# Performance work log

Measured on AMD Instinct MI355X. Metric: run time of the kernel, lower is better.

Reference implementation:

```python
import jax, jax.numpy as jnp
import numpy as np

B, L, D, F, T = 32, 768, 256, 256, 3072
_EPS = 1e-5


def _layernorm(h, g, b):
    mu = jnp.mean(h, axis=-1, keepdims=True)
    var = jnp.var(h, axis=-1, keepdims=True)
    return (h - mu) * jax.lax.rsqrt(var + _EPS) * g + b


def _conv1d(h, w, b):
    # h: [B, L, Cin], w: [K, Cin, Cout] (HIO), padding=1 matches torch Conv1d(padding=1)
    return jax.lax.conv_general_dilated(h, w, (1,), [(1, 1)], dimension_numbers=('NHC', 'HIO', 'NHC')) + b


def setup_inputs() -> dict:
    key = jax.random.key(0)
    ks = jax.random.split(key, 6)
    return {
        'x': jax.random.normal(ks[0], (B, L, D), jnp.float32),
        'target': jax.random.randint(ks[1], (B, L), 0, 4, jnp.int32),
        'mel_max_length': T,
        'conv1_w': jax.random.normal(ks[2], (3, D, F), jnp.float32) * 0.05,
        'conv1_b': jnp.zeros((F,), jnp.float32),
        'ln1_g': jnp.ones((F,), jnp.float32),
        'ln1_b': jnp.zeros((F,), jnp.float32),
        'conv2_w': jax.random.normal(ks[3], (3, F, F), jnp.float32) * 0.05,
        'conv2_b': jnp.zeros((F,), jnp.float32),
        'ln2_g': jnp.ones((F,), jnp.float32),
        'ln2_b': jnp.zeros((F,), jnp.float32),
        'lin_w': jax.random.normal(ks[4], (F, 1), jnp.float32) * 0.05,
        'lin_b': jnp.zeros((1,), jnp.float32),
    }


def reference(x, target, mel_max_length, conv1_w, conv1_b, ln1_g, ln1_b,
              conv2_w, conv2_b, ln2_g, ln2_b, lin_w, lin_b):
    alpha = 1.0
    # DurationPredictor: conv -> relu -> LN -> conv -> relu -> LN -> linear (dropout=0)
    h = _layernorm(jax.nn.relu(_conv1d(x, conv1_w, conv1_b)), ln1_g, ln1_b)
    h = _layernorm(jax.nn.relu(_conv1d(h, conv2_w, conv2_b)), ln2_g, ln2_b)
    dp_out = (h @ lin_w + lin_b)[..., 0]                       # [B, L]
    durations = jnp.exp(dp_out) * alpha                        # [B, L] float
    # Training branch: durations come from target
    dpo = jnp.round(target.astype(jnp.float32) * alpha).astype(jnp.int32)  # [B, L]
    # LR: alignment @ x realized as cumulative-duration searchsorted + gather
    cum = jnp.cumsum(dpo, axis=1)                              # [B, L]
    t = jnp.arange(mel_max_length, dtype=jnp.int32)            # [T]
    idx = jax.vmap(lambda c: jnp.searchsorted(c, t, side='right'))(cum)  # [B, T]
    mask = (t[None, :] < cum[:, -1:]).astype(x.dtype)          # [B, T] zero past total frames
    out = jnp.take_along_axis(x, jnp.clip(idx, 0, x.shape[1] - 1)[:, :, None], axis=1)
    out = out * mask[:, :, None]                               # [B, T, D]
    return (out, dpo, durations)
```

## Files before the change

kernel.cpp:

```cpp
#include <hip/hip_runtime.h>
#include <hip/hip_bf16.h>
#include <math.h>

#define BB 32
#define LL 768
#define DD 256
#define FF 256
#define TT 3072
#define MT 48
#define PAD 262
#define A1R 66

typedef __attribute__((ext_vector_type(8))) short bf16x8;
typedef __attribute__((ext_vector_type(4))) float f32x4;

__device__ inline unsigned short f2b(float f) {
    union { float f; unsigned u; } v; v.f = f;
    unsigned r = (v.u + 0x7FFF + ((v.u >> 16) & 1)) >> 16;
    return (unsigned short)r;
}

__device__ inline unsigned cvt_pk_bf16(float lo, float hi) {
    unsigned r;
    asm("v_cvt_pk_bf16_f32 %0, %1, %2" : "=v"(r) : "v"(lo), "v"(hi));
    return r;
}

#define DPP_ROR_ADD(v, ctrl)                                                   \
    v += __int_as_float(__builtin_amdgcn_update_dpp(                           \
        0, __float_as_int(v), ctrl, 0xF, 0xF, false))

__device__ inline void red16_pair(float& a, float& b) {
    DPP_ROR_ADD(a, 0x128); DPP_ROR_ADD(b, 0x128);
    DPP_ROR_ADD(a, 0x124); DPP_ROR_ADD(b, 0x124);
    DPP_ROR_ADD(a, 0x122); DPP_ROR_ADD(b, 0x122);
    DPP_ROR_ADD(a, 0x121); DPP_ROR_ADD(b, 0x121);
}

__device__ inline float red16_one(float a) {
    DPP_ROR_ADD(a, 0x128);
    DPP_ROR_ADD(a, 0x124);
    DPP_ROR_ADD(a, 0x122);
    DPP_ROR_ADD(a, 0x121);
    return a;
}

__global__ __launch_bounds__(256) void prep_scan_kernel(
    const float* __restrict__ w1, const float* __restrict__ w2,
    unsigned short* __restrict__ wQ1, unsigned short* __restrict__ wQ2,
    const int* __restrict__ target,
    float* __restrict__ out_dpo,
    int* __restrict__ idx_map)
{
    __shared__ int tsum[256];
    const int tid = threadIdx.x;

    if (blockIdx.x < 48) {
        const int layer = blockIdx.x / 24;
        const int s  = blockIdx.x % 24;
        const int kc = s >> 3, c8 = s & 7;
        const float* __restrict__ w = layer ? w2 : w1;
        unsigned short* __restrict__ o = (layer ? wQ2 : wQ1) + s * 8192 + tid * 32;
        const int n = tid;

        alignas(16) unsigned short tmp[32];
#pragma unroll
        for (int q = 0; q < 4; ++q)
#pragma unroll
            for (int j = 0; j < 8; ++j) {
                const int cin = c8 * 32 + q * 8 + j;
                tmp[q * 8 + j] = f2b(w[((size_t)(kc * 256 + cin)) * 256 + n]);
            }
#pragma unroll
        for (int i = 0; i < 4; ++i)
            *reinterpret_cast<uint4*>(o + i * 8) = *reinterpret_cast<const uint4*>(tmp + i * 8);
        return;
    }

    const int b = blockIdx.x - 48;

    const int l = 3 * tid;
    const int v0 = target[b * LL + l];
    const int v1 = target[b * LL + l + 1];
    const int v2 = target[b * LL + l + 2];
    out_dpo[b * LL + l]     = (float)v0;
    out_dpo[b * LL + l + 1] = (float)v1;
    out_dpo[b * LL + l + 2] = (float)v2;

    const int s0 = v0, s1 = v0 + v1, s2 = v0 + v1 + v2;
    tsum[tid] = s2;
    __syncthreads();
    for (int off = 1; off < 256; off <<= 1) {
        int xq = (tid >= off) ? tsum[tid - off] : 0;
        __syncthreads();
        tsum[tid] += xq;
        __syncthreads();
    }
    const int excl = tsum[tid] - s2;

    for (int t = tid; t < TT; t += 256) idx_map[b * TT + t] = -1;
    __syncthreads();

    const int c0 = excl + s0, c1 = excl + s1, c2 = excl + s2;
    for (int t = excl; t < c0 && t < TT; ++t) idx_map[b * TT + t] = l;
    for (int t = c0;   t < c1 && t < TT; ++t) idx_map[b * TT + t] = l + 1;
    for (int t = c1;   t < c2 && t < TT; ++t) idx_map[b * TT + t] = l + 2;
}

__global__ __launch_bounds__(256, 2) void fused_dp_kernel(
    const float* __restrict__ x,
    const unsigned short* __restrict__ wQ1,
    const unsigned short* __restrict__ wQ2,
    const float* __restrict__ c1b, const float* __restrict__ g1, const float* __restrict__ b1,
    const float* __restrict__ c2b, const float* __restrict__ g2, const float* __restrict__ b2,
    const float* __restrict__ lw,  const float* __restrict__ lb,
    float* __restrict__ out_dur)
{
    __shared__ union {
        unsigned short A1[A1R * PAD];
        unsigned short h2[50 * PAD];
    } sm;
    __shared__ float red[4][4][4][4][2];
    __shared__ float redp[4][3][4][4];
    __shared__ float fin[50][2];

    const int tid  = threadIdx.x;
    const int b    = blockIdx.x / (LL / MT);
    const int l0   = (blockIdx.x % (LL / MT)) * MT;
    const int wave = tid >> 6, lane = tid & 63;
    const int quad = lane >> 4, l16 = lane & 15;

    int   cols[4];
    float c1bv[4], g1v[4], b1v[4], c2bv[4], g2v[4], b2v[4], lwv[4];
#pragma unroll
    for (int nt = 0; nt < 4; ++nt) {
        const int c = wave * 64 + nt * 16 + l16;
        cols[nt] = c;
        c1bv[nt] = c1b[c]; g1v[nt] = g1[c]; b1v[nt] = b1[c];
        c2bv[nt] = c2b[c]; g2v[nt] = g2[c]; b2v[nt] = b2[c];
        lwv[nt]  = lw[c];
    }
    const float lbv = lb[0];

    {
        float4 v0[7], v1[7];
        int lr[7];
#pragma unroll
        for (int k = 0; k < 7; ++k) {
            const int q  = tid + (k << 8);
            const int ar = q >> 5;
            const int l  = l0 - 2 + ar;
            lr[k] = (ar < 52 && l >= 0 && l < LL) ? l : -1;
            if (lr[k] >= 0) {
                const float* pp = x + ((size_t)b * LL + lr[k]) * DD + (q & 31) * 8;
                v0[k] = *reinterpret_cast<const float4*>(pp);
                v1[k] = *reinterpret_cast<const float4*>(pp + 4);
            }
        }
#pragma unroll
        for (int k = 0; k < 7; ++k) {
            const int q  = tid + (k << 8);
            const int ar = q >> 5;
            uint4 uu = {0u, 0u, 0u, 0u};
            if (lr[k] >= 0) {
                uu.x = cvt_pk_bf16(v0[k].x, v0[k].y);
                uu.y = cvt_pk_bf16(v0[k].z, v0[k].w);
                uu.z = cvt_pk_bf16(v1[k].x, v1[k].y);
                uu.w = cvt_pk_bf16(v1[k].z, v1[k].w);
            }
            *reinterpret_cast<uint4*>(&sm.A1[ar * PAD + (q & 31) * 8]) = uu;
        }
        for (int q = tid; q < 320; q += 256) {
            const int ar = 56 + (q >> 5);
            uint4 z = {0u, 0u, 0u, 0u};
            *reinterpret_cast<uint4*>(&sm.A1[ar * PAD + (q & 31) * 8]) = z;
        }
    }
    __syncthreads();

    f32x4 acc1[4][4] = {};
    {
        bf16x8 aE[4], bE[4], aO[4], bO[4];
        auto ld1 = [&](bf16x8* a, bf16x8* bf, int s) {
            const int kc = s >> 3, c8 = s & 7;
#pragma unroll
            for (int nt = 0; nt < 4; ++nt)
                bf[nt] = *reinterpret_cast<const bf16x8*>(
                    wQ1 + (size_t)s * 8192 + cols[nt] * 32 + quad * 8);
#pragma unroll
            for (int mt = 0; mt < 4; ++mt)
                a[mt] = *reinterpret_cast<const bf16x8*>(
                    &sm.A1[(16 * mt + l16 + kc) * PAD + c8 * 32 + quad * 8]);
        };
        auto mm1 = [&](bf16x8* a, bf16x8* bf) {
            __builtin_amdgcn_s_setprio(1);
#pragma unroll
            for (int mt = 0; mt < 4; ++mt)
#pragma unroll
                for (int nt = 0; nt < 4; ++nt)
                    acc1[mt][nt] = __builtin_amdgcn_mfma_f32_16x16x32_bf16(
                        a[mt], bf[nt], acc1[mt][nt], 0, 0, 0);
            __builtin_amdgcn_s_setprio(0);
        };
        ld1(aE, bE, 0);
        for (int s = 0; s < 24; s += 2) {
            ld1(aO, bO, s + 1);
            mm1(aE, bE);
            if (s + 2 < 24) ld1(aE, bE, s + 2);
            mm1(aO, bO);
        }
    }
    __syncthreads();

#pragma unroll
    for (int mt = 0; mt < 4; ++mt)
#pragma unroll
        for (int r = 0; r < 4; ++r) {
            float s1 = 0.f, s2 = 0.f;
#pragma unroll
            for (int nt = 0; nt < 4; ++nt) {
                const float v = fmaxf(acc1[mt][nt][r] + c1bv[nt], 0.f);
                s1 += v; s2 += v * v;
            }
            red16_pair(s1, s2);
            if (l16 == 0) { red[wave][mt][quad][r][0] = s1; red[wave][mt][quad][r][1] = s2; }
        }
    __syncthreads();
    if (tid < 50) {
        const int mt = tid >> 4, q = (tid >> 2) & 3, r = tid & 3;
        const float s1 = red[0][mt][q][r][0] + red[1][mt][q][r][0]
                       + red[2][mt][q][r][0] + red[3][mt][q][r][0];
        const float s2 = red[0][mt][q][r][1] + red[1][mt][q][r][1]
                       + red[2][mt][q][r][1] + red[3][mt][q][r][1];
        const float mu  = s1 * (1.f / 256.f);
        const float var = s2 * (1.f / 256.f) - mu * mu;
        fin[tid][0] = mu;
        fin[tid][1] = rsqrtf(var + 1e-5f);
    }
    __syncthreads();

#pragma unroll
    for (int mt = 0; mt < 4; ++mt)
#pragma unroll
        for (int r = 0; r < 4; ++r) {
            const int rho = 16 * mt + quad * 4 + r;
            if (rho < 50) {
                const int gr = l0 - 1 + rho;
                const float mu = fin[rho][0], rstd = fin[rho][1];
#pragma unroll
                for (int nt = 0; nt < 4; ++nt) {
                    unsigned short hv = 0;
                    if (gr >= 0 && gr < LL) {
                        const float v = fmaxf(acc1[mt][nt][r] + c1bv[nt], 0.f);
                        hv = f2b((v - mu) * rstd * g1v[nt] + b1v[nt]);
                    }
                    sm.h2[rho * PAD + cols[nt]] = hv;
                }
            }
        }
    __syncthreads();

    f32x4 acc2[3][4] = {};
    {
        bf16x8 aE[3], bE[4], aO[3], bO[4];
        auto ld2 = [&](bf16x8* a, bf16x8* bf, int s) {
            const int kc = s >> 3, c8 = s & 7;
#pragma unroll
            for (int nt = 0; nt < 4; ++nt)
                bf[nt] = *reinterpret_cast<const bf16x8*>(
                    wQ2 + (size_t)s * 8192 + cols[nt] * 32 + quad * 8);
#pragma unroll
            for (int mt = 0; mt < 3; ++mt)
                a[mt] = *reinterpret_cast<const bf16x8*>(
                    &sm.h2[(16 * mt + l16 + kc) * PAD + c8 * 32 + quad * 8]);
        };
        auto mm2 = [&](bf16x8* a, bf16x8* bf) {
            __builtin_amdgcn_s_setprio(1);
#pragma unroll
            for (int mt = 0; mt < 3; ++mt)
#pragma unroll
                for (int nt = 0; nt < 4; ++nt)
                    acc2[mt][nt] = __builtin_amdgcn_mfma_f32_16x16x32_bf16(
                        a[mt], bf[nt], acc2[mt][nt], 0, 0, 0);
            __builtin_amdgcn_s_setprio(0);
        };
        ld2(aE, bE, 0);
        for (int s = 0; s < 24; s += 2) {
            ld2(aO, bO, s + 1);
            mm2(aE, bE);
            if (s + 2 < 24) ld2(aE, bE, s + 2);
            mm2(aO, bO);
        }
    }

#pragma unroll
    for (int mt = 0; mt < 3; ++mt)
#pragma unroll
        for (int r = 0; r < 4; ++r) {
            float s1 = 0.f, s2 = 0.f;
#pragma unroll
            for (int nt = 0; nt < 4; ++nt) {
                const float v = fmaxf(acc2[mt][nt][r] + c2bv[nt], 0.f);
                s1 += v; s2 += v * v;
            }
            red16_pair(s1, s2);
            if (l16 == 0) { red[wave][mt][quad][r][0] = s1; red[wave][mt][quad][r][1] = s2; }
        }
    __syncthreads();
    if (tid < MT) {
        const int mt = tid >> 4, q = (tid >> 2) & 3, r = tid & 3;
        const float s1 = red[0][mt][q][r][0] + red[1][mt][q][r][0]
                       + red[2][mt][q][r][0] + red[3][mt][q][r][0];
        const float s2 = red[0][mt][q][r][1] + red[1][mt][q][r][1]
                       + red[2][mt][q][r][1] + red[3][mt][q][r][1];
        const float mu  = s1 * (1.f / 256.f);
        const float var = s2 * (1.f / 256.f) - mu * mu;
        fin[tid][0] = mu;
        fin[tid][1] = rsqrtf(var + 1e-5f);
    }
    __syncthreads();

#pragma unroll
    for (int mt = 0; mt < 3; ++mt)
#pragma unroll
        for (int r = 0; r < 4; ++r) {
            const int rho = 16 * mt + quad * 4 + r;
            const float mu = fin[rho][0], rstd = fin[rho][1];
            float p = 0.f;
#pragma unroll
            for (int nt = 0; nt < 4; ++nt) {
                const float v = fmaxf(acc2[mt][nt][r] + c2bv[nt], 0.f);
                p += ((v - mu) * rstd * g2v[nt] + b2v[nt]) * lwv[nt];
            }
            p = red16_one(p);
            if (l16 == 0) redp[wave][mt][quad][r] = p;
        }
    __syncthreads();
    if (tid < MT) {
        const int mt = tid >> 4, q = (tid >> 2) & 3, r = tid & 3;
        const float dp = redp[0][mt][q][r] + redp[1][mt][q][r]
                       + redp[2][mt][q][r] + redp[3][mt][q][r] + lbv;
        out_dur[(size_t)b * LL + l0 + tid] = expf(dp);
    }
}

__global__ __launch_bounds__(256) void gather_kernel(
    const float* __restrict__ x,
    const int* __restrict__ idx_map,
    float* __restrict__ out)
{
    const int wv = threadIdx.x >> 6, lane = threadIdx.x & 63;
    const int row = blockIdx.x * 4 + wv;
    const int b = row / TT, t = row - b * TT;
    const int idx = idx_map[b * TT + t];
    f32x4 val = {0.f, 0.f, 0.f, 0.f};
    if (idx >= 0)
        val = *reinterpret_cast<const f32x4*>(x + ((size_t)(b * LL + idx)) * DD + lane * 4);
    __builtin_nontemporal_store(val, reinterpret_cast<f32x4*>(out) + (size_t)row * (DD / 4) + lane);
}

extern "C" void kernel_launch(void* const* d_in, const int* in_sizes, int n_in,
                              void* d_out, int out_size, void* d_ws, size_t ws_size,
                              hipStream_t stream)
{
    const float* x      = (const float*)d_in[0];
    const int*   target = (const int*)  d_in[1];
    const float* c1w = (const float*)d_in[3];
    const float* c1b = (const float*)d_in[4];
    const float* g1  = (const float*)d_in[5];
    const float* b1  = (const float*)d_in[6];
    const float* c2w = (const float*)d_in[7];
    const float* c2b = (const float*)d_in[8];
    const float* g2  = (const float*)d_in[9];
    const float* b2  = (const float*)d_in[10];
    const float* lw  = (const float*)d_in[11];
    const float* lb  = (const float*)d_in[12];

    float* out0    = (float*)d_out;
    float* out_dpo = out0 + (size_t)BB * TT * DD;
    float* out_dur = out_dpo + (size_t)BB * LL;

    char* ws = (char*)d_ws;
    unsigned short* wQ1 = (unsigned short*)ws;                 ws += (size_t)24 * 8192 * 2;
    unsigned short* wQ2 = (unsigned short*)ws;                 ws += (size_t)24 * 8192 * 2;
    int* idx_map        = (int*)ws;

    prep_scan_kernel<<<48 + BB, 256, 0, stream>>>(
        c1w, c2w, wQ1, wQ2, target, out_dpo, idx_map);

    fused_dp_kernel<<<BB * (LL / MT), 256, 0, stream>>>(
        x, wQ1, wQ2, c1b, g1, b1, c2b, g2, b2, lw, lb, out_dur);

    gather_kernel<<<BB * TT / 4, 256, 0, stream>>>(x, idx_map, out0);
}
```

Before: 193.3 us.

## Load conv1 A operands directly from global, drop LDS staging and prefetch conv2 weights

The first conv's input tile is no longer staged through shared memory. Each wave loads fp32 rows of x straight from global inside the K loop, converts them to bf16 in registers and feeds them to MFMA with software pipelining. This removes the LDS write, a barrier and the shared union. The second conv's weight loads are issued before the barrier and the loop is re-pipelined, so weights arrive earlier. The cost is redundant global reads of x across the four waves and more registers in flight, which could reduce occupancy.

```diff
diff --git a/kernel.cpp b/kernel.cpp
--- a/kernel.cpp
+++ b/kernel.cpp
@@ -9,7 +9,6 @@
 #define TT 3072
 #define MT 48
 #define PAD 262
-#define A1R 66
 
 typedef __attribute__((ext_vector_type(8))) short bf16x8;
 typedef __attribute__((ext_vector_type(4))) float f32x4;
@@ -116,10 +115,7 @@
     const float* __restrict__ lw,  const float* __restrict__ lb,
     float* __restrict__ out_dur)
 {
-    __shared__ union {
-        unsigned short A1[A1R * PAD];
-        unsigned short h2[50 * PAD];
-    } sm;
+    __shared__ unsigned short h2[50 * PAD];
     __shared__ float red[4][4][4][4][2];
     __shared__ float redp[4][3][4][4];
     __shared__ float fin[50][2];
@@ -142,55 +138,39 @@
     }
     const float lbv = lb[0];
 
-    {
-        float4 v0[7], v1[7];
-        int lr[7];
-#pragma unroll
-        for (int k = 0; k < 7; ++k) {
-            const int q  = tid + (k << 8);
-            const int ar = q >> 5;
-            const int l  = l0 - 2 + ar;
-            lr[k] = (ar < 52 && l >= 0 && l < LL) ? l : -1;
-            if (lr[k] >= 0) {
-                const float* pp = x + ((size_t)b * LL + lr[k]) * DD + (q & 31) * 8;
-                v0[k] = *reinterpret_cast<const float4*>(pp);
-                v1[k] = *reinterpret_cast<const float4*>(pp + 4);
-            }
-        }
-#pragma unroll
-        for (int k = 0; k < 7; ++k) {
-            const int q  = tid + (k << 8);
-            const int ar = q >> 5;
-            uint4 uu = {0u, 0u, 0u, 0u};
-            if (lr[k] >= 0) {
-                uu.x = cvt_pk_bf16(v0[k].x, v0[k].y);
-                uu.y = cvt_pk_bf16(v0[k].z, v0[k].w);
-                uu.z = cvt_pk_bf16(v1[k].x, v1[k].y);
-                uu.w = cvt_pk_bf16(v1[k].z, v1[k].w);
-            }
-            *reinterpret_cast<uint4*>(&sm.A1[ar * PAD + (q & 31) * 8]) = uu;
-        }
-        for (int q = tid; q < 320; q += 256) {
-            const int ar = 56 + (q >> 5);
-            uint4 z = {0u, 0u, 0u, 0u};
-            *reinterpret_cast<uint4*>(&sm.A1[ar * PAD + (q & 31) * 8]) = z;
-        }
-    }
-    __syncthreads();
-
     f32x4 acc1[4][4] = {};
     {
         bf16x8 aE[4], bE[4], aO[4], bO[4];
-        auto ld1 = [&](bf16x8* a, bf16x8* bf, int s) {
+        float4 r0[4], r1[4];
+        auto issue1 = [&](bf16x8* bf, int s) {
             const int kc = s >> 3, c8 = s & 7;
+#pragma unroll
+            for (int mt = 0; mt < 4; ++mt) {
+                const int ar = 16 * mt + l16 + kc;
+                const int l  = l0 - 2 + ar;
+                float4 z = {0.f, 0.f, 0.f, 0.f};
+                r0[mt] = z; r1[mt] = z;
+                if (ar < 52 && l >= 0 && l < LL) {
+                    const float* pp = x + ((size_t)b * LL + l) * DD + c8 * 32 + quad * 8;
+                    r0[mt] = *reinterpret_cast<const float4*>(pp);
+                    r1[mt] = *reinterpret_cast<const float4*>(pp + 4);
+                }
+            }
 #pragma unroll
             for (int nt = 0; nt < 4; ++nt)
                 bf[nt] = *reinterpret_cast<const bf16x8*>(
                     wQ1 + (size_t)s * 8192 + cols[nt] * 32 + quad * 8);
-#pragma unroll
-            for (int mt = 0; mt < 4; ++mt)
-                a[mt] = *reinterpret_cast<const bf16x8*>(
-                    &sm.A1[(16 * mt + l16 + kc) * PAD + c8 * 32 + quad * 8]);
+        };
+        auto cvt1 = [&](bf16x8* a) {
+#pragma unroll
+            for (int mt = 0; mt < 4; ++mt) {
+                union { unsigned u[4]; bf16x8 v; } t;
+                t.u[0] = cvt_pk_bf16(r0[mt].x, r0[mt].y);
+                t.u[1] = cvt_pk_bf16(r0[mt].z, r0[mt].w);
+                t.u[2] = cvt_pk_bf16(r1[mt].x, r1[mt].y);
+                t.u[3] = cvt_pk_bf16(r1[mt].z, r1[mt].w);
+                a[mt] = t.v;
+            }
         };
         auto mm1 = [&](bf16x8* a, bf16x8* bf) {
             __builtin_amdgcn_s_setprio(1);
@@ -202,15 +182,17 @@
                         a[mt], bf[nt], acc1[mt][nt], 0, 0, 0);
             __builtin_amdgcn_s_setprio(0);
         };
-        ld1(aE, bE, 0);
+        issue1(bE, 0);
+        cvt1(aE);
         for (int s = 0; s < 24; s += 2) {
-            ld1(aO, bO, s + 1);
+            issue1(bO, s + 1);
             mm1(aE, bE);
-            if (s + 2 < 24) ld1(aE, bE, s + 2);
+            cvt1(aO);
+            if (s + 2 < 24) issue1(bE, s + 2);
             mm1(aO, bO);
-        }
-    }
-    __syncthreads();
+            if (s + 2 < 24) cvt1(aE);
+        }
+    }
 
 #pragma unroll
     for (int mt = 0; mt < 4; ++mt)
@@ -254,26 +236,31 @@
                         const float v = fmaxf(acc1[mt][nt][r] + c1bv[nt], 0.f);
                         hv = f2b((v - mu) * rstd * g1v[nt] + b1v[nt]);
                     }
-                    sm.h2[rho * PAD + cols[nt]] = hv;
+                    h2[rho * PAD + cols[nt]] = hv;
                 }
             }
         }
+
+    bf16x8 aE2[3], bE2[4], aO2[3], bO2[4];
+    auto ldb2 = [&](bf16x8* bf, int s) {
+#pragma unroll
+        for (int nt = 0; nt < 4; ++nt)
+            bf[nt] = *reinterpret_cast<const bf16x8*>(
+                wQ2 + (size_t)s * 8192 + cols[nt] * 32 + quad * 8);
+    };
+    auto lda2 = [&](bf16x8* a, int s) {
+        const int kc = s >> 3, c8 = s & 7;
+#pragma unroll
+        for (int mt = 0; mt < 3; ++mt)
+            a[mt] = *reinterpret_cast<const bf16x8*>(
+                &h2[(16 * mt + l16 + kc) * PAD + c8 * 32 + quad * 8]);
+    };
+    ldb2(bE2, 0);
+    ldb2(bO2, 1);
     __syncthreads();
 
     f32x4 acc2[3][4] = {};
     {
-        bf16x8 aE[3], bE[4], aO[3], bO[4];
-        auto ld2 = [&](bf16x8* a, bf16x8* bf, int s) {
-            const int kc = s >> 3, c8 = s & 7;
-#pragma unroll
-            for (int nt = 0; nt < 4; ++nt)
-                bf[nt] = *reinterpret_cast<const bf16x8*>(
-                    wQ2 + (size_t)s * 8192 + cols[nt] * 32 + quad * 8);
-#pragma unroll
-            for (int mt = 0; mt < 3; ++mt)
-                a[mt] = *reinterpret_cast<const bf16x8*>(
-                    &sm.h2[(16 * mt + l16 + kc) * PAD + c8 * 32 + quad * 8]);
-        };
         auto mm2 = [&](bf16x8* a, bf16x8* bf) {
             __builtin_amdgcn_s_setprio(1);
 #pragma unroll
@@ -284,12 +271,13 @@
                         a[mt], bf[nt], acc2[mt][nt], 0, 0, 0);
             __builtin_amdgcn_s_setprio(0);
         };
-        ld2(aE, bE, 0);
+        lda2(aE2, 0);
         for (int s = 0; s < 24; s += 2) {
-            ld2(aO, bO, s + 1);
-            mm2(aE, bE);
-            if (s + 2 < 24) ld2(aE, bE, s + 2);
-            mm2(aO, bO);
+            lda2(aO2, s + 1);
+            mm2(aE2, bE2);
+            if (s + 2 < 24) { ldb2(bE2, s + 2); lda2(aE2, s + 2); }
+            mm2(aO2, bO2);
+            if (s + 3 < 24) ldb2(bO2, s + 3);
         }
     }
 
```

Measured after the change: 208.6 us. 7.9% more time.
